# Optimization experiments

Measured on AMD Instinct MI355X. Metric: run time of the kernel, lower is better.

## Reference

```python
import jax, jax.numpy as jnp
import numpy as np

SCALING = 32.0 / 16  # alpha / r

def setup_inputs() -> dict:
    key = jax.random.key(0)
    k = jax.random.split(key, 7)
    d_in, d_out, r = 4096, 4096, 16
    x = jax.random.normal(k[0], (4, 2048, d_in), dtype=jnp.float32)
    # int4 symmetric codes in [-8, 7], stored as int32 (int8 semantics)
    qweight = jax.random.randint(k[1], (d_out, d_in), -8, 8, dtype=jnp.int32)
    # per-row quantized scale in [1, 127] (scale > 0 in the torch module)
    qscale = jax.random.randint(k[2], (d_out, 1), 1, 128, dtype=jnp.int32)
    meta_scale = jax.random.uniform(k[3], (), dtype=jnp.float32) * 0.01 + 1e-4
    bias = jax.random.normal(k[4], (d_out,), dtype=jnp.float32)
    lora_A = jax.random.normal(k[5], (r, d_in), dtype=jnp.float32) * (1.0 / np.sqrt(d_in))
    lora_B = jax.random.normal(k[6], (d_out, r), dtype=jnp.float32) * 0.02
    return {"x": x, "qweight": qweight, "qscale": qscale, "meta_scale": meta_scale,
            "bias": bias, "lora_A": lora_A, "lora_B": lora_B}

def reference(x, qweight, qscale, meta_scale, bias, lora_A, lora_B):
    # Two-level dequant: W[o,i] = qweight[o,i] * (qscale[o] * meta_scale)
    scale_row = qscale.astype(jnp.float32) * meta_scale        # [d_out, 1]
    W = qweight.astype(jnp.float32) * scale_row                # [d_out, d_in]
    W = W.astype(x.dtype)
    # base linear: x @ W^T + b
    out = jnp.einsum('bsi,oi->bso', x, W) + bias
    # LoRA low-rank update (dropout p=0 -> identity)
    xA = jnp.einsum('bsi,ri->bsr', x, lora_A.astype(x.dtype))  # [b, s, r]
    xAB = jnp.einsum('bsr,or->bso', xA, lora_B.astype(x.dtype))
    return out + SCALING * xAB
```

## Files before the change

### kernel.cpp

```cpp
#include <hip/hip_runtime.h>
#include <hip/hip_bf16.h>
#include <stdint.h>

typedef short   s16x8  __attribute__((ext_vector_type(8)));
typedef float   f32x4a __attribute__((ext_vector_type(4)));
typedef int     i32x4v __attribute__((ext_vector_type(4)));
typedef unsigned short u16x4 __attribute__((ext_vector_type(4)));
typedef int     i32x4  __attribute__((ext_vector_type(4)));

#define D_IN   4096
#define D_OUT  4096
#define RANK   16
#define MROWS  8192
#define NTI    32

__device__ __forceinline__ uint16_t f32_to_bf16(float f) {
  union { float f; uint32_t u; } v; v.f = f;
  uint32_t u = v.u;
  return (uint16_t)((u + 0x7FFFu + ((u >> 16) & 1u)) >> 16);
}

__device__ __forceinline__ void gload16(void* lds, const void* g) {
  __builtin_amdgcn_global_load_lds(
      (const __attribute__((address_space(1))) uint32_t*)g,
      (__attribute__((address_space(3))) uint32_t*)lds, 16, 0, 0);
}

extern "C" __global__ __launch_bounds__(256) void k_prep(
    const float* __restrict__ x, const int* __restrict__ qw,
    const float* __restrict__ loraA, const float* __restrict__ loraB,
    signed char* __restrict__ xq, float* __restrict__ sx,
    signed char* __restrict__ wq, uint16_t* __restrict__ lb16,
    uint16_t* __restrict__ lab) {
  const int bid = blockIdx.x, tid = threadIdx.x;
  if (bid < 2048) {
    const int w = tid >> 6, l = tid & 63;
    const int64_t row = (int64_t)bid * 4 + w;
    const f32x4a* xr = (const f32x4a*)(x + row * D_IN);
    f32x4a v[16];
    float m = 0.f;
#pragma unroll
    for (int i = 0; i < 16; ++i) {
      v[i] = xr[i * 64 + l];
#pragma unroll
      for (int j = 0; j < 4; ++j) m = fmaxf(m, fabsf(v[i][j]));
    }
#pragma unroll
    for (int off = 32; off > 0; off >>= 1)
      m = fmaxf(m, __shfl_xor(m, off));
    m = fmaxf(m, 1e-20f);
    const float s = m / 127.f, rs = 127.f / m;
    int* qrow = (int*)(xq + row * D_IN);
#pragma unroll
    for (int i = 0; i < 16; ++i) {
      int b = 0;
#pragma unroll
      for (int j = 0; j < 4; ++j) {
        float t = fminf(fmaxf(rintf(v[i][j] * rs), -127.f), 127.f);
        b |= ((int)t & 255) << (8 * j);
      }
      __builtin_nontemporal_store(b, qrow + i * 64 + l);
    }
    if (l == 0) sx[row] = s;
  } else {
    const int wb = bid - 2048;
#pragma unroll
    for (int r = 0; r < 4; ++r) {
      const int n = wb * 4 + r;
      const int* row = qw + (int64_t)n * D_IN + tid * 16;
      i32x4 o;
#pragma unroll
      for (int j = 0; j < 4; j++) {
        i32x4 u = *(const i32x4*)(row + j * 4);
        o[j] = (u[0] & 255) | ((u[1] & 255) << 8) | ((u[2] & 255) << 16)
             | (u[3] << 24);
      }
      __builtin_nontemporal_store(o,
          (i32x4*)(wq + (int64_t)n * D_IN + tid * 16));
      if (tid < RANK)
        lb16[n * RANK + tid] = f32_to_bf16(2.0f * loraB[n * RANK + tid]);
      if (n < RANK) {
        const float* ar = loraA + (int64_t)n * D_IN + tid * 16;
        uint16_t*    lr = lab   + (int64_t)n * D_IN + tid * 16;
        u16x4 q;
#pragma unroll
        for (int j = 0; j < 4; ++j) {
          f32x4a u = *(const f32x4a*)(ar + j * 4);
#pragma unroll
          for (int e = 0; e < 4; ++e) q[e] = f32_to_bf16(u[e]);
          *(u16x4*)(lr + j * 4) = q;
        }
      }
    }
  }
}

extern "C" __global__ __launch_bounds__(64) void k_xa(
    const signed char* __restrict__ xq, const float* __restrict__ sx,
    const uint16_t* __restrict__ lab, uint16_t* __restrict__ xa) {
  const int l = threadIdx.x;
  const int l15 = l & 15, lk = l >> 4;
  const int64_t row0 = (int64_t)blockIdx.x * 16;
  f32x4a acc = {0.f, 0.f, 0.f, 0.f};
  const signed char* xrow = xq + (row0 + l15) * D_IN + lk * 8;
  const uint16_t*    arow = lab + (int64_t)l15 * D_IN + lk * 8;
#pragma unroll 4
  for (int k0 = 0; k0 < D_IN; k0 += 32) {
    int64_t vv = *(const int64_t*)(xrow + k0);
    s16x8 bf = *(const s16x8*)(arow + k0);
    s16x8 af;
#pragma unroll
    for (int j = 0; j < 8; ++j) {
      signed char c = (signed char)(vv >> (8 * j));
      af[j] = (short)f32_to_bf16((float)c);
    }
    acc = __builtin_amdgcn_mfma_f32_16x16x32_bf16(af, bf, acc, 0, 0, 0);
  }
#pragma unroll
  for (int reg = 0; reg < 4; reg++) {
    int64_t mr = row0 + lk * 4 + reg;
    xa[mr * RANK + l15] = f32_to_bf16(acc[reg] * sx[mr]);
  }
}

extern "C" __global__ __launch_bounds__(512, 2) void k_gemm(
    const signed char* __restrict__ A, const signed char* __restrict__ B,
    const float* __restrict__ sx, const int* __restrict__ qscale,
    const float* __restrict__ meta, const float* __restrict__ bias,
    const uint16_t* __restrict__ xa, const uint16_t* __restrict__ lb16,
    float* __restrict__ out) {
  extern __shared__ char ldsc[];
  char* aB = ldsc;
  char* bB = ldsc + 65536;

  const int tid = threadIdx.x;
  const int bid = blockIdx.x;
  const int xcd = bid & 7, loc = bid >> 3;
  const int mtile = xcd * 4 + (loc & 3);
  const int ntile = loc >> 2;

  const int w = tid >> 6, l = tid & 63;
  const int wm = w >> 2, wn = w & 3;
  const int l15 = l & 15, lk = l >> 4;
  const int fro = lk * 256 + l15 * 16;

  const signed char* Ag = A + (int64_t)mtile * 256 * D_IN;
  const signed char* Bg = B + (int64_t)ntile * 256 * D_IN;

  const int row_lo = ((tid >> 6) << 4) | (tid & 15);
  const int64_t s_lo = (int64_t)row_lo * D_IN + ((tid >> 4) & 3) * 16;
  const int64_t s_hi = s_lo + (int64_t)128 * D_IN;

#define STG_K0(bufp, gp, kb) {                                      \
    gload16((bufp) + (size_t)tid * 16,        (gp) + (kb) + s_lo);  \
    gload16((bufp) + (size_t)(512 + tid) * 16,(gp) + (kb) + s_hi); }
#define STG_K1(bufp, gp, kb) {                                           \
    gload16((bufp) + (size_t)(1024 + tid) * 16,(gp) + (kb) + 64 + s_lo); \
    gload16((bufp) + (size_t)(1536 + tid) * 16,(gp) + (kb) + 64 + s_hi); }

  i32x4v acc[8][4];
#pragma unroll
  for (int i = 0; i < 8; i++)
#pragma unroll
    for (int j = 0; j < 4; j++) acc[i][j] = (i32x4v){0, 0, 0, 0};

  STG_K0(aB, Ag, 0); STG_K0(bB, Bg, 0);
  STG_K1(aB, Ag, 0); STG_K1(bB, Bg, 0);
  asm volatile("s_waitcnt vmcnt(4)" ::: "memory");
  asm volatile("s_barrier" ::: "memory");

  i32x4v bf[4];

#define PHASE(MH, KC, STAGE_STMT, WAIT_STMT) {                               \
    i32x4v af[4];                                                            \
    _Pragma("unroll")                                                        \
    for (int mi = 0; mi < 4; ++mi)                                           \
      af[mi] = *(const i32x4v*)(cA + (KC) * 16384 +                          \
                                (wm * 8 + (MH) * 4 + mi) * 1024 + fro);      \
    if ((MH) == 0) {                                                         \
      _Pragma("unroll")                                                      \
      for (int ni = 0; ni < 4; ++ni)                                         \
        bf[ni] = *(const i32x4v*)(cB + (KC) * 16384 +                        \
                                  (wn * 4 + ni) * 1024 + fro);               \
    }                                                                        \
    STAGE_STMT;                                                              \
    asm volatile("s_barrier" ::: "memory");                                  \
    asm volatile("s_waitcnt lgkmcnt(0)" ::: "memory");                       \
    __builtin_amdgcn_s_setprio(1);                                           \
    _Pragma("unroll")                                                        \
    for (int mi = 0; mi < 4; ++mi)                                           \
      _Pragma("unroll")                                                      \
      for (int ni = 0; ni < 4; ++ni)                                         \
        acc[(MH) * 4 + mi][ni] = __builtin_amdgcn_mfma_i32_16x16x64_i8(      \
            af[mi], bf[ni], acc[(MH) * 4 + mi][ni], 0, 0, 0);                \
    __builtin_amdgcn_s_setprio(0);                                           \
    WAIT_STMT;                                                               \
    asm volatile("s_barrier" ::: "memory"); }

  for (int kt = 0; kt < NTI; ++kt) {
    const int cur = kt & 1;
    const char* cA = aB + cur * 32768;
    const char* cB = bB + cur * 32768;
    char* nA = aB + (cur ^ 1) * 32768;
    char* nB = bB + (cur ^ 1) * 32768;
    const int64_t kb = (int64_t)(kt + 1) * 128;
    const bool full = (kt < NTI - 1);

    PHASE(0, 0, if (full) STG_K0(nA, Ag, kb), )
    PHASE(1, 0, if (full) STG_K0(nB, Bg, kb),
          if (full) { asm volatile("s_waitcnt vmcnt(4)" ::: "memory"); }
          else      { asm volatile("s_waitcnt vmcnt(0)" ::: "memory"); })
    PHASE(0, 1, if (full) STG_K1(nA, Ag, kb), )
    PHASE(1, 1, if (full) STG_K1(nB, Bg, kb),
          if (full) { asm volatile("s_waitcnt vmcnt(4)" ::: "memory"); })
  }

  const float mv = meta[0];
  const int64_t mrow0 = (int64_t)mtile * 256 + wm * 128;
  const int ncol0 = ntile * 256 + wn * 64;

  s16x8 xf[8];
#pragma unroll
  for (int mi = 0; mi < 8; ++mi) {
    xf[mi] = (s16x8){0, 0, 0, 0, 0, 0, 0, 0};
    if (lk < 2)
      xf[mi] = *(const s16x8*)(xa + (mrow0 + mi * 16 + l15) * RANK + lk * 8);
  }
  s16x8 lbf[4];
#pragma unroll
  for (int ni = 0; ni < 4; ++ni) {
    lbf[ni] = (s16x8){0, 0, 0, 0, 0, 0, 0, 0};
    if (lk < 2)
      lbf[ni] = *(const s16x8*)(lb16 + (ncol0 + ni * 16 + l15) * RANK + lk * 8);
  }
  float sxv[8][4];
#pragma unroll
  for (int mi = 0; mi < 8; ++mi)
#pragma unroll
    for (int reg = 0; reg < 4; reg++)
      sxv[mi][reg] = sx[mrow0 + mi * 16 + lk * 4 + reg];

#pragma unroll
  for (int ni = 0; ni < 4; ++ni) {
    int n = ncol0 + ni * 16 + l15;
    float sr = (float)qscale[n] * mv;
    float bv = bias[n];
#pragma unroll
    for (int mi = 0; mi < 8; ++mi) {
      f32x4a lf = {0.f, 0.f, 0.f, 0.f};
      lf = __builtin_amdgcn_mfma_f32_16x16x32_bf16(xf[mi], lbf[ni], lf, 0, 0, 0);
      float* op = out + (mrow0 + mi * 16 + lk * 4) * (int64_t)D_OUT + n;
#pragma unroll
      for (int reg = 0; reg < 4; reg++)
        __builtin_nontemporal_store(
            (float)acc[mi][ni][reg] * (sxv[mi][reg] * sr) + lf[reg] + bv,
            op + (int64_t)reg * D_OUT);
    }
  }
#undef PHASE
#undef STG_K0
#undef STG_K1
}

extern "C" void kernel_launch(void* const* d_in, const int* in_sizes, int n_in,
                              void* d_out, int out_size, void* d_ws, size_t ws_size,
                              hipStream_t stream) {
  const float* x    = (const float*)d_in[0];
  const int*   qw   = (const int*)d_in[1];
  const int*   qs   = (const int*)d_in[2];
  const float* meta = (const float*)d_in[3];
  const float* bias = (const float*)d_in[4];
  const float* lA   = (const float*)d_in[5];
  const float* lB   = (const float*)d_in[6];
  float* out = (float*)d_out;

  signed char* xq   = (signed char*)d_ws;
  signed char* wq   = xq + (size_t)MROWS * D_IN;
  float*       sx   = (float*)(wq + (size_t)D_OUT * D_IN);
  uint16_t*    xa   = (uint16_t*)(sx + MROWS);
  uint16_t*    lb16 = xa + (size_t)MROWS * RANK;
  uint16_t*    lab  = lb16 + (size_t)D_OUT * RANK;
  const size_t need = (size_t)MROWS * D_IN + (size_t)D_OUT * D_IN +
                      MROWS * 4 + (size_t)MROWS * RANK * 2 +
                      (size_t)D_OUT * RANK * 2 + (size_t)RANK * D_IN * 2;
  if (ws_size < need) return;

  const int lds_bytes = 131072;
  (void)hipFuncSetAttribute((const void*)k_gemm,
                            hipFuncAttributeMaxDynamicSharedMemorySize,
                            lds_bytes);

  k_prep<<<2048 + D_OUT / 4, 256, 0, stream>>>(x, qw, lA, lB, xq, sx, wq,
                                               lb16, lab);
  k_xa<<<MROWS / 16, 64, 0, stream>>>(xq, sx, lab, xa);
  k_gemm<<<512, 512, lds_bytes, stream>>>(xq, wq, sx, qs, meta, bias,
                                          xa, lb16, out);
}
```

Measured before the change: 253.0 us.

## Regroup prep kernels so weight conversion overlaps the xA LoRA projection

The prep work is split differently. The first kernel now quantizes x and converts lora_A. The second kernel converts the int32 weights and lora_B in some blocks and computes xA with 4-wave blocks in the others, so the weight conversion runs alongside the xA MFMA work instead of in front of it. Nontemporal stores are replaced with regular stores, so xq and wq may stay in L2 for the next kernels. The kernel count stays at three, but the block shapes and the load balance change.

```diff
diff --git a/kernel.cpp b/kernel.cpp
--- a/kernel.cpp
+++ b/kernel.cpp
@@ -26,47 +26,64 @@
       (__attribute__((address_space(3))) uint32_t*)lds, 16, 0, 0);
 }
 
-extern "C" __global__ __launch_bounds__(256) void k_prep(
-    const float* __restrict__ x, const int* __restrict__ qw,
-    const float* __restrict__ loraA, const float* __restrict__ loraB,
+extern "C" __global__ __launch_bounds__(256) void k_quant_x(
+    const float* __restrict__ x, const float* __restrict__ loraA,
     signed char* __restrict__ xq, float* __restrict__ sx,
-    signed char* __restrict__ wq, uint16_t* __restrict__ lb16,
     uint16_t* __restrict__ lab) {
   const int bid = blockIdx.x, tid = threadIdx.x;
-  if (bid < 2048) {
-    const int w = tid >> 6, l = tid & 63;
-    const int64_t row = (int64_t)bid * 4 + w;
-    const f32x4a* xr = (const f32x4a*)(x + row * D_IN);
-    f32x4a v[16];
-    float m = 0.f;
-#pragma unroll
-    for (int i = 0; i < 16; ++i) {
-      v[i] = xr[i * 64 + l];
-#pragma unroll
-      for (int j = 0; j < 4; ++j) m = fmaxf(m, fabsf(v[i][j]));
-    }
-#pragma unroll
-    for (int off = 32; off > 0; off >>= 1)
-      m = fmaxf(m, __shfl_xor(m, off));
-    m = fmaxf(m, 1e-20f);
-    const float s = m / 127.f, rs = 127.f / m;
-    int* qrow = (int*)(xq + row * D_IN);
-#pragma unroll
-    for (int i = 0; i < 16; ++i) {
-      int b = 0;
-#pragma unroll
-      for (int j = 0; j < 4; ++j) {
-        float t = fminf(fmaxf(rintf(v[i][j] * rs), -127.f), 127.f);
-        b |= ((int)t & 255) << (8 * j);
-      }
-      __builtin_nontemporal_store(b, qrow + i * 64 + l);
-    }
-    if (l == 0) sx[row] = s;
-  } else {
-    const int wb = bid - 2048;
+  const int w = tid >> 6, l = tid & 63;
+  const int64_t row = (int64_t)bid * 4 + w;
+  const f32x4a* xr = (const f32x4a*)(x + row * D_IN);
+  f32x4a v[16];
+  float m = 0.f;
+#pragma unroll
+  for (int i = 0; i < 16; ++i) {
+    v[i] = xr[i * 64 + l];
+#pragma unroll
+    for (int j = 0; j < 4; ++j) m = fmaxf(m, fabsf(v[i][j]));
+  }
+#pragma unroll
+  for (int off = 32; off > 0; off >>= 1)
+    m = fmaxf(m, __shfl_xor(m, off));
+  m = fmaxf(m, 1e-20f);
+  const float s = m / 127.f, rs = 127.f / m;
+  int* qrow = (int*)(xq + row * D_IN);
+#pragma unroll
+  for (int i = 0; i < 16; ++i) {
+    int b = 0;
+#pragma unroll
+    for (int j = 0; j < 4; ++j) {
+      float t = fminf(fmaxf(rintf(v[i][j] * rs), -127.f), 127.f);
+      b |= ((int)t & 255) << (8 * j);
+    }
+    qrow[i * 64 + l] = b;
+  }
+  if (l == 0) sx[row] = s;
+
+  if (bid < RANK) {
+    const float* ar = loraA + (int64_t)bid * D_IN + tid * 16;
+    uint16_t*    lr = lab   + (int64_t)bid * D_IN + tid * 16;
+    u16x4 q;
+#pragma unroll
+    for (int j = 0; j < 4; ++j) {
+      f32x4a u = *(const f32x4a*)(ar + j * 4);
+#pragma unroll
+      for (int e = 0; e < 4; ++e) q[e] = f32_to_bf16(u[e]);
+      *(u16x4*)(lr + j * 4) = q;
+    }
+  }
+}
+
+extern "C" __global__ __launch_bounds__(256) void k_convw_xa(
+    const int* __restrict__ qw, const float* __restrict__ loraB,
+    const signed char* __restrict__ xq, const float* __restrict__ sx,
+    const uint16_t* __restrict__ lab, signed char* __restrict__ wq,
+    uint16_t* __restrict__ lb16, uint16_t* __restrict__ xa) {
+  const int bid = blockIdx.x, tid = threadIdx.x;
+  if (bid < 1024) {
 #pragma unroll
     for (int r = 0; r < 4; ++r) {
-      const int n = wb * 4 + r;
+      const int n = bid * 4 + r;
       const int* row = qw + (int64_t)n * D_IN + tid * 16;
       i32x4 o;
 #pragma unroll
@@ -75,51 +92,34 @@
         o[j] = (u[0] & 255) | ((u[1] & 255) << 8) | ((u[2] & 255) << 16)
              | (u[3] << 24);
       }
-      __builtin_nontemporal_store(o,
-          (i32x4*)(wq + (int64_t)n * D_IN + tid * 16));
+      *(i32x4*)(wq + (int64_t)n * D_IN + tid * 16) = o;
       if (tid < RANK)
         lb16[n * RANK + tid] = f32_to_bf16(2.0f * loraB[n * RANK + tid]);
-      if (n < RANK) {
-        const float* ar = loraA + (int64_t)n * D_IN + tid * 16;
-        uint16_t*    lr = lab   + (int64_t)n * D_IN + tid * 16;
-        u16x4 q;
-#pragma unroll
-        for (int j = 0; j < 4; ++j) {
-          f32x4a u = *(const f32x4a*)(ar + j * 4);
-#pragma unroll
-          for (int e = 0; e < 4; ++e) q[e] = f32_to_bf16(u[e]);
-          *(u16x4*)(lr + j * 4) = q;
-        }
+    }
+  } else {
+    const int w = tid >> 6, l = tid & 63;
+    const int l15 = l & 15, lk = l >> 4;
+    const int64_t row0 = (int64_t)(bid - 1024) * 64 + w * 16;
+    f32x4a acc = {0.f, 0.f, 0.f, 0.f};
+    const signed char* xrow = xq + (row0 + l15) * D_IN + lk * 8;
+    const uint16_t*    arow = lab + (int64_t)l15 * D_IN + lk * 8;
+#pragma unroll 4
+    for (int k0 = 0; k0 < D_IN; k0 += 32) {
+      int64_t vv = *(const int64_t*)(xrow + k0);
+      s16x8 bf = *(const s16x8*)(arow + k0);
+      s16x8 af;
+#pragma unroll
+      for (int j = 0; j < 8; ++j) {
+        signed char c = (signed char)(vv >> (8 * j));
+        af[j] = (short)f32_to_bf16((float)c);
       }
-    }
-  }
-}
-
-extern "C" __global__ __launch_bounds__(64) void k_xa(
-    const signed char* __restrict__ xq, const float* __restrict__ sx,
-    const uint16_t* __restrict__ lab, uint16_t* __restrict__ xa) {
-  const int l = threadIdx.x;
-  const int l15 = l & 15, lk = l >> 4;
-  const int64_t row0 = (int64_t)blockIdx.x * 16;
-  f32x4a acc = {0.f, 0.f, 0.f, 0.f};
-  const signed char* xrow = xq + (row0 + l15) * D_IN + lk * 8;
-  const uint16_t*    arow = lab + (int64_t)l15 * D_IN + lk * 8;
-#pragma unroll 4
-  for (int k0 = 0; k0 < D_IN; k0 += 32) {
-    int64_t vv = *(const int64_t*)(xrow + k0);
-    s16x8 bf = *(const s16x8*)(arow + k0);
-    s16x8 af;
-#pragma unroll
-    for (int j = 0; j < 8; ++j) {
-      signed char c = (signed char)(vv >> (8 * j));
-      af[j] = (short)f32_to_bf16((float)c);
-    }
-    acc = __builtin_amdgcn_mfma_f32_16x16x32_bf16(af, bf, acc, 0, 0, 0);
-  }
-#pragma unroll
-  for (int reg = 0; reg < 4; reg++) {
-    int64_t mr = row0 + lk * 4 + reg;
-    xa[mr * RANK + l15] = f32_to_bf16(acc[reg] * sx[mr]);
+      acc = __builtin_amdgcn_mfma_f32_16x16x32_bf16(af, bf, acc, 0, 0, 0);
+    }
+#pragma unroll
+    for (int reg = 0; reg < 4; reg++) {
+      int64_t mr = row0 + lk * 4 + reg;
+      xa[mr * RANK + l15] = f32_to_bf16(acc[reg] * sx[mr]);
+    }
   }
 }
 
@@ -290,9 +290,9 @@
                             hipFuncAttributeMaxDynamicSharedMemorySize,
                             lds_bytes);
 
-  k_prep<<<2048 + D_OUT / 4, 256, 0, stream>>>(x, qw, lA, lB, xq, sx, wq,
-                                               lb16, lab);
-  k_xa<<<MROWS / 16, 64, 0, stream>>>(xq, sx, lab, xa);
+  k_quant_x<<<MROWS / 4, 256, 0, stream>>>(x, lA, xq, sx, lab);
+  k_convw_xa<<<1024 + MROWS / 64, 256, 0, stream>>>(qw, lB, xq, sx, lab,
+                                                    wq, lb16, xa);
   k_gemm<<<512, 512, lds_bytes, stream>>>(xq, wq, sx, qs, meta, bias,
                                           xa, lb16, out);
 }
```

Measured after the change: 235.8 us. -6.8%, faster.
